# Kernel tuning notes

Hardware: AMD Instinct MI355X
Metric: run time of the kernel (lower is better)

## Reference

```python
import jax, jax.numpy as jnp
import numpy as np

N = 4096
NFEAT = 1024
NHID = 512
NCLS = 32
NLAYERS = 3
SPARSITY = 0.002


def _l2norm(x, eps=1e-12):
    n = jnp.sqrt(jnp.sum(x * x, axis=1, keepdims=True))
    return x / jnp.maximum(n, eps)


def setup_inputs() -> dict:
    key = jax.random.key(0)
    ks = jax.random.split(key, 12)
    # sparse-valued dense adjacency (original stores torch.sparse but densifies every hop)
    vals = jax.random.uniform(ks[0], (N, N), dtype=jnp.float32)
    mask = jax.random.uniform(ks[1], (N, N)) < SPARSITY
    adj = jnp.where(mask, vals, 0.0)
    features = jax.random.normal(ks[2], (N, NFEAT), dtype=jnp.float32)
    # y is a one-hot label matrix [N, nclass]
    labels = jax.random.randint(ks[3], (N,), 0, NCLS)
    y = jax.nn.one_hot(labels, NCLS, dtype=jnp.float32)
    s = 0.02
    W0 = jax.random.normal(ks[4], (NFEAT + 3 * NCLS, NHID), dtype=jnp.float32) * s
    b0 = jnp.zeros((NHID,), jnp.float32)
    W1_0 = jax.random.normal(ks[5], (NHID + 3 * NCLS, NHID), dtype=jnp.float32) * s
    b1_0 = jnp.zeros((NHID,), jnp.float32)
    W1_1 = jax.random.normal(ks[6], (NHID + 3 * NCLS, NHID), dtype=jnp.float32) * s
    b1_1 = jnp.zeros((NHID,), jnp.float32)
    W2 = jax.random.normal(ks[7], (NFEAT + NHID, NCLS), dtype=jnp.float32) * s
    b2 = jnp.zeros((NCLS,), jnp.float32)
    alphas = jnp.ones((NLAYERS, 5), jnp.float32)
    return {
        "adj": adj, "features": features, "y": y,
        "W0": W0, "b0": b0, "W1_0": W1_0, "b1_0": b1_0,
        "W1_1": W1_1, "b1_1": b1_1, "W2": W2, "b2": b2,
        "alphas": alphas, "layer_norm": 1,
    }


def reference(adj, features, y, W0, b0, W1_0, b1_0, W1_1, b1_1, W2, b2, alphas, layer_norm):
    Ws = [(W0, b0), (W1_0, b1_0), (W1_1, b1_1)]
    initial_features = jax.lax.stop_gradient(features)  # .clone().detach()
    feats = features
    max_features = None
    pow_adj = adj  # persists across layers (faithful to original): hops adj, adj^2, adj^4
    for i in range(NLAYERS):
        mask_alpha = jax.nn.softmax(alphas[i], axis=0)
        for _ in range(i):
            pow_adj = adj @ pow_adj
        hop = pow_adj @ feats                                   # [N, d]
        dist = (pow_adj > 0).astype(adj.dtype)                  # binarized reachability
        y_out = dist @ y                                        # [N, c]
        y_in = dist.T @ y                                       # [N, c]
        y_all = y_in + y_out
        hop = mask_alpha[0] * hop
        y_out = mask_alpha[1] * y_out
        y_in = mask_alpha[2] * y_in
        y_all = mask_alpha[3] * y_all
        mat = jnp.concatenate([hop, y_out, y_in, y_all], axis=1)
        W, b = Ws[i]
        tmp = mat @ W + b
        if layer_norm:
            tmp = _l2norm(tmp)
        feats = tmp
        max_features = tmp if max_features is None else jnp.maximum(max_features, tmp)
    final_mat = jnp.concatenate([initial_features, max_features], axis=1)
    out = jax.nn.relu(final_mat)
    # dropout: eval mode (identity)
    out = out @ W2 + b2
    return jax.nn.log_softmax(out, axis=1)
```

## Files before the change

kernel.cpp:

```cpp
#include <hip/hip_runtime.h>
#include <hip/hip_bf16.h>
#include <math.h>

typedef unsigned long long u64;
typedef unsigned short ushort_t;
typedef float f32x4 __attribute__((ext_vector_type(4)));
typedef short s16x8 __attribute__((ext_vector_type(8)));

#define NN 4096
#define NF 1024
#define NH 512
#define NC 32
#define LDP 40

__device__ inline float bf2f(ushort_t u) {
    unsigned int v = ((unsigned int)u) << 16;
    return __uint_as_float(v);
}
__device__ inline ushort_t f2bf(float f) {
    __hip_bfloat16 h = __float2bfloat16(f);
    return *(ushort_t*)&h;
}

__device__ void role_build(int i, int l, const float* __restrict__ adj,
                           u64* __restrict__ B1, int* __restrict__ rowcnt,
                           int* __restrict__ colidx, float* __restrict__ vals) {
    const float* row = adj + (size_t)i * NN + l * 64;
    const float4* row4 = (const float4*)row;
    u64 w = 0;
    #pragma unroll
    for (int k = 0; k < 16; ++k) {
        float4 v = row4[k];
        if (v.x > 0.f) w |= 1ULL << (4*k + 0);
        if (v.y > 0.f) w |= 1ULL << (4*k + 1);
        if (v.z > 0.f) w |= 1ULL << (4*k + 2);
        if (v.w > 0.f) w |= 1ULL << (4*k + 3);
    }
    B1[(size_t)i*64 + l] = w;
    int cnt = __popcll(w);
    int pre = cnt;
    #pragma unroll
    for (int o = 1; o < 64; o <<= 1) {
        int u = __shfl_up(pre, o, 64);
        if (l >= o) pre += u;
    }
    int excl = pre - cnt;
    int total = __shfl(pre, 63, 64);
    u64 ww = w;
    int idx = excl;
    while (ww) {
        int b = __ffsll((unsigned long long)ww) - 1;
        ww &= ww - 1;
        if (idx < 64) {
            colidx[i*64 + idx] = l*64 + b;
            vals[i*64 + idx] = row[b];
        }
        ++idx;
    }
    int tot = total < 64 ? total : 64;
    for (int s = tot + l; s < 64; s += 64) {
        colidx[i*64 + s] = 0;
        vals[i*64 + s] = 0.f;
    }
    if (l == 0) {
        int r8 = (tot + 7) & ~7;
        rowcnt[i] = r8 < 64 ? r8 : 64;
    }
}

__device__ void role_wt(const float* __restrict__ W, ushort_t* __restrict__ Wt,
                        int ksrc0, int Kd, int idx, char* smem, int t) {
    float (*tile)[33] = (float(*)[33])smem;
    int ktiles = Kd >> 5;
    int kb = (idx % ktiles) * 32, nb = (idx / ktiles) * 32;
    int tc = t & 31, tr8 = t >> 5;
    for (int r = tr8; r < 32; r += 8)
        tile[r][tc] = W[(size_t)(ksrc0 + kb + r) * NH + nb + tc];
    __syncthreads();
    for (int r = tr8; r < 32; r += 8)
        Wt[(size_t)(nb + r) * Kd + kb + tc] = f2bf(tile[tc][r]);
}

__device__ void role_bsq(int i, int t, char* smem, const u64* __restrict__ Bidx,
                         const u64* __restrict__ Bdat, u64* __restrict__ Bout) {
    u64* ridx = (u64*)smem;
    u64* part = ridx + 64;
    int wid = t >> 6, lane = t & 63;
    if (t < 64) ridx[t] = Bidx[(size_t)i*64 + t];
    __syncthreads();
    u64 acc = 0;
    for (int u = wid*16; u < wid*16 + 16; ++u) {
        u64 w = ridx[u];
        while (w) {
            int k = u*64 + (__ffsll((unsigned long long)w) - 1);
            w &= (w - 1);
            acc |= Bdat[(size_t)k*64 + lane];
        }
    }
    part[wid*64 + lane] = acc;
    __syncthreads();
    if (t < 64) Bout[(size_t)i*64 + t] = part[t] | part[64+t] | part[128+t] | part[192+t];
}

__device__ void role_btrans(int tb, int wid, int l, char* smem,
                            const u64* __restrict__ B, u64* __restrict__ BT) {
    u64* ld = ((u64*)smem) + wid*64;
    int I = tb >> 6, J = tb & 63;
    ld[l] = B[(size_t)(I*64 + l)*64 + J];
    __syncthreads();
    u64 out = 0;
    #pragma unroll
    for (int r = 0; r < 64; ++r) out |= ((ld[r] >> l) & 1ULL) << r;
    BT[(size_t)(J*64 + l)*64 + I] = out;
}

__device__ void role_ymat(int rb, int t, char* smem, const u64* __restrict__ B,
                          const u64* __restrict__ BT, const u64* __restrict__ LC,
                          const float* __restrict__ asp, ushort_t* __restrict__ yc) {
    u64* LCt   = (u64*)smem;
    u64* rows  = LCt + 64*32;
    u64* rowsT = rows + 8*64;
    for (int k = t; k < 2048; k += 256) {
        int c = k >> 6, w = k & 63;
        LCt[w*32 + c] = LC[k];
    }
    for (int k = t; k < 512; k += 256) {
        int r = k >> 6, w = k & 63;
        rows[r*64 + w]  = B[(size_t)(rb + r)*64 + w];
        rowsT[r*64 + w] = BT[(size_t)(rb + r)*64 + w];
    }
    __syncthreads();
    int wid = t >> 6, lane = t & 63;
    int h = lane >> 5, c = lane & 31;
    int r = wid * 2 + h;
    int co = 0, ci = 0;
    #pragma unroll
    for (int w = 0; w < 64; ++w) {
        u64 lc = LCt[w*32 + c];
        co += __popcll(rows[r*64 + w]  & lc);
        ci += __popcll(rowsT[r*64 + w] & lc);
    }
    float a1 = asp[1], a2 = asp[2], a3 = asp[3];
    size_t i = rb + r;
    yc[i*96 + c]      = f2bf(a1 * (float)co);
    yc[i*96 + 32 + c] = f2bf(a2 * (float)ci);
    yc[i*96 + 64 + c] = f2bf(a3 * (float)(co + ci));
}

__device__ void role_gemm(int bx, int tid, char* smem, const ushort_t* __restrict__ Abf,
                          const float* __restrict__ Af, int Ka,
                          const ushort_t* __restrict__ Bt, int K,
                          ushort_t* __restrict__ Cb, float* __restrict__ Cf) {
    ushort_t* As = (ushort_t*)smem;
    ushort_t* Bs = As + 64*LDP;
    int xcd = bx & 7, rest = bx >> 3;
    int nt = rest & 7, mt = (rest >> 3) * 8 + xcd;
    int bm = mt * 64, bn = nt * 64;
    int srow = tid >> 2, scol = (tid & 3) * 8;
    int wid = tid >> 6, lane = tid & 63;
    int fr = lane & 15, hi2 = lane >> 4, fk = hi2 * 8;
    f32x4 acc[4] = {{0,0,0,0},{0,0,0,0},{0,0,0,0},{0,0,0,0}};
    for (int k0 = 0; k0 < K; k0 += 32) {
        if (Abf) {
            *(s16x8*)&As[srow * LDP + scol] =
                *(const s16x8*)&Abf[(size_t)(bm + srow) * Ka + k0 + scol];
        } else {
            const float* ap = &Af[(size_t)(bm + srow) * Ka + k0 + scol];
            float4 a0 = *(const float4*)ap;
            float4 a1 = *(const float4*)(ap + 4);
            s16x8 o;
            o[0] = (short)f2bf(a0.x); o[1] = (short)f2bf(a0.y);
            o[2] = (short)f2bf(a0.z); o[3] = (short)f2bf(a0.w);
            o[4] = (short)f2bf(a1.x); o[5] = (short)f2bf(a1.y);
            o[6] = (short)f2bf(a1.z); o[7] = (short)f2bf(a1.w);
            *(s16x8*)&As[srow * LDP + scol] = o;
        }
        *(s16x8*)&Bs[srow * LDP + scol] =
            *(const s16x8*)&Bt[(size_t)(bn + srow) * K + k0 + scol];
        __syncthreads();
        s16x8 af = *(const s16x8*)&As[(wid * 16 + fr) * LDP + fk];
        #pragma unroll
        for (int j = 0; j < 4; ++j) {
            s16x8 bfv = *(const s16x8*)&Bs[(j * 16 + fr) * LDP + fk];
            acc[j] = __builtin_amdgcn_mfma_f32_16x16x32_bf16(af, bfv, acc[j], 0, 0, 0);
        }
        __syncthreads();
    }
    int drow = bm + wid * 16 + hi2 * 4;
    #pragma unroll
    for (int j = 0; j < 4; ++j) {
        int col = bn + j * 16 + fr;
        #pragma unroll
        for (int r = 0; r < 4; ++r) {
            if (Cb) Cb[(size_t)(drow + r) * NH + col] = f2bf(acc[j][r]);
            else    Cf[(size_t)(drow + r) * NH + col] = acc[j][r];
        }
    }
}

__device__ void role_spmm(int i, int lane, const int* __restrict__ rc,
                          const int* __restrict__ ci, const float* __restrict__ vl,
                          const ushort_t* __restrict__ X, ushort_t* __restrict__ Y) {
    int cnt = rc[i];
    float acc[8] = {0,0,0,0,0,0,0,0};
    for (int p = 0; p < cnt; p += 8) {
        int4   c0 = *(const int4*)&ci[i*64 + p];
        int4   c1 = *(const int4*)&ci[i*64 + p + 4];
        float4 v0 = *(const float4*)&vl[i*64 + p];
        float4 v1 = *(const float4*)&vl[i*64 + p + 4];
        s16x8 x0 = *(const s16x8*)&X[(size_t)c0.x * NH + 8*lane];
        s16x8 x1 = *(const s16x8*)&X[(size_t)c0.y * NH + 8*lane];
        s16x8 x2 = *(const s16x8*)&X[(size_t)c0.z * NH + 8*lane];
        s16x8 x3 = *(const s16x8*)&X[(size_t)c0.w * NH + 8*lane];
        s16x8 x4 = *(const s16x8*)&X[(size_t)c1.x * NH + 8*lane];
        s16x8 x5 = *(const s16x8*)&X[(size_t)c1.y * NH + 8*lane];
        s16x8 x6 = *(const s16x8*)&X[(size_t)c1.z * NH + 8*lane];
        s16x8 x7 = *(const s16x8*)&X[(size_t)c1.w * NH + 8*lane];
        #pragma unroll
        for (int j = 0; j < 8; ++j) {
            acc[j] += v0.x * bf2f((ushort_t)x0[j]);
            acc[j] += v0.y * bf2f((ushort_t)x1[j]);
            acc[j] += v0.z * bf2f((ushort_t)x2[j]);
            acc[j] += v0.w * bf2f((ushort_t)x3[j]);
            acc[j] += v1.x * bf2f((ushort_t)x4[j]);
            acc[j] += v1.y * bf2f((ushort_t)x5[j]);
            acc[j] += v1.z * bf2f((ushort_t)x6[j]);
            acc[j] += v1.w * bf2f((ushort_t)x7[j]);
        }
    }
    s16x8 o;
    #pragma unroll
    for (int j = 0; j < 8; ++j) o[j] = (short)f2bf(acc[j]);
    *(s16x8*)&Y[(size_t)i*NH + 8*lane] = o;
}

__device__ void role_spmmF(int i, int lane, const int* __restrict__ rc,
                           const int* __restrict__ ci, const float* __restrict__ vl,
                           const ushort_t* __restrict__ X, const float* __restrict__ yv,
                           const float* __restrict__ bias, int ln, float alpha,
                           ushort_t* __restrict__ F) {
    int cnt = rc[i];
    float acc[8] = {0,0,0,0,0,0,0,0};
    for (int p = 0; p < cnt; p += 8) {
        int4   c0 = *(const int4*)&ci[i*64 + p];
        int4   c1 = *(const int4*)&ci[i*64 + p + 4];
        float4 v0 = *(const float4*)&vl[i*64 + p];
        float4 v1 = *(const float4*)&vl[i*64 + p + 4];
        s16x8 x0 = *(const s16x8*)&X[(size_t)c0.x * NH + 8*lane];
        s16x8 x1 = *(const s16x8*)&X[(size_t)c0.y * NH + 8*lane];
        s16x8 x2 = *(const s16x8*)&X[(size_t)c0.z * NH + 8*lane];
        s16x8 x3 = *(const s16x8*)&X[(size_t)c0.w * NH + 8*lane];
        s16x8 x4 = *(const s16x8*)&X[(size_t)c1.x * NH + 8*lane];
        s16x8 x5 = *(const s16x8*)&X[(size_t)c1.y * NH + 8*lane];
        s16x8 x6 = *(const s16x8*)&X[(size_t)c1.z * NH + 8*lane];
        s16x8 x7 = *(const s16x8*)&X[(size_t)c1.w * NH + 8*lane];
        #pragma unroll
        for (int j = 0; j < 8; ++j) {
            acc[j] += v0.x * bf2f((ushort_t)x0[j]);
            acc[j] += v0.y * bf2f((ushort_t)x1[j]);
            acc[j] += v0.z * bf2f((ushort_t)x2[j]);
            acc[j] += v0.w * bf2f((ushort_t)x3[j]);
            acc[j] += v1.x * bf2f((ushort_t)x4[j]);
            acc[j] += v1.y * bf2f((ushort_t)x5[j]);
            acc[j] += v1.z * bf2f((ushort_t)x6[j]);
            acc[j] += v1.w * bf2f((ushort_t)x7[j]);
        }
    }
    const float* yr = yv + (size_t)i * NH + 8*lane;
    float4 ya = *(const float4*)yr;
    float4 yb = *(const float4*)(yr + 4);
    float4 ba = *(const float4*)&bias[8*lane];
    float4 bb = *(const float4*)&bias[8*lane + 4];
    float v[8];
    v[0] = alpha*acc[0] + ya.x + ba.x; v[1] = alpha*acc[1] + ya.y + ba.y;
    v[2] = alpha*acc[2] + ya.z + ba.z; v[3] = alpha*acc[3] + ya.w + ba.w;
    v[4] = alpha*acc[4] + yb.x + bb.x; v[5] = alpha*acc[5] + yb.y + bb.y;
    v[6] = alpha*acc[6] + yb.z + bb.z; v[7] = alpha*acc[7] + yb.w + bb.w;
    float ss = 0.f;
    #pragma unroll
    for (int j = 0; j < 8; ++j) ss += v[j]*v[j];
    #pragma unroll
    for (int o = 1; o < 64; o <<= 1) ss += __shfl_xor(ss, o, 64);
    float sc = ln ? 1.0f / fmaxf(sqrtf(ss), 1e-12f) : 1.0f;
    s16x8 o;
    #pragma unroll
    for (int j = 0; j < 8; ++j) o[j] = (short)f2bf(v[j] * sc);
    *(s16x8*)&F[(size_t)i*NH + 8*lane] = o;
}

__global__ __launch_bounds__(256) void k_setup(const float* __restrict__ adj,
        const float* __restrict__ features, ushort_t* __restrict__ featb,
        const float* __restrict__ y, u64* __restrict__ LC,
        const float* __restrict__ W0, const float* __restrict__ W1_0,
        const float* __restrict__ W1_1,
        ushort_t* __restrict__ Wh0t, ushort_t* __restrict__ Wy0t,
        ushort_t* __restrict__ Wh1t, ushort_t* __restrict__ Wy1t,
        ushort_t* __restrict__ Wh2t, ushort_t* __restrict__ Wy2t,
        const float* __restrict__ alphas, float* __restrict__ a_sm,
        u64* __restrict__ B1, int* __restrict__ rowcnt,
        int* __restrict__ colidx, float* __restrict__ vals) {
    __shared__ __align__(16) char smem[4352];
    int b = blockIdx.x, t = threadIdx.x;
    int wid = t >> 6, l = t & 63;
    if (b < 1024) {
        role_build(b*4 + wid, l, adj, B1, rowcnt, colidx, vals);
    } else if (b < 5120) {
        int base = (b - 1024) * 1024 + t * 4;
        float4 v = *(const float4*)&features[base];
        ushort4 o;
        o.x = f2bf(v.x); o.y = f2bf(v.y); o.z = f2bf(v.z); o.w = f2bf(v.w);
        *(ushort4*)&featb[base] = o;
    } else if (b < 5136) {
        int w = (b - 5120) * 4 + wid;
        const float* yr = y + (size_t)(w*64 + l) * NC;
        for (int c = 0; c < NC; ++c) {
            u64 m = __ballot(yr[c] > 0.5f);
            if (l == c) LC[c*64 + w] = m;
        }
    } else if (b < 5648) { role_wt(W0,   Wh0t, 0,    NF, b - 5136, smem, t); }
    else if (b < 5696)   { role_wt(W0,   Wy0t, NF,   96, b - 5648, smem, t); }
    else if (b < 5952)   { role_wt(W1_0, Wh1t, 0,    NH, b - 5696, smem, t); }
    else if (b < 6000)   { role_wt(W1_0, Wy1t, NH,   96, b - 5952, smem, t); }
    else if (b < 6256)   { role_wt(W1_1, Wh2t, 0,    NH, b - 6000, smem, t); }
    else if (b < 6304)   { role_wt(W1_1, Wy2t, NH,   96, b - 6256, smem, t); }
    else {
        if (t == 0) {
            for (int i = 0; i < 3; ++i) {
                float m = -1e30f;
                for (int j = 0; j < 5; ++j) m = fmaxf(m, alphas[i*5+j]);
                float e[5]; float s = 0.f;
                for (int j = 0; j < 5; ++j) { e[j] = expf(alphas[i*5+j] - m); s += e[j]; }
                for (int j = 0; j < 5; ++j) a_sm[i*5+j] = e[j] / s;
            }
        }
    }
}

__global__ __launch_bounds__(256) void k_p2(const ushort_t* __restrict__ featb,
        const ushort_t* __restrict__ Wh0t, ushort_t* __restrict__ zb,
        const u64* __restrict__ B1, u64* __restrict__ B2, u64* __restrict__ B1T) {
    __shared__ __align__(16) char smem[10240];
    int b = blockIdx.x, t = threadIdx.x;
    int wid = t >> 6, l = t & 63;
    if (b < 512)       role_gemm(b, t, smem, featb, nullptr, NF, Wh0t, NF, zb, nullptr);
    else if (b < 4608) role_bsq(b - 512, t, smem, B1, B1, B2);
    else               role_btrans((b - 4608)*4 + wid, wid, l, smem, B1, B1T);
}

__global__ __launch_bounds__(256) void k_p3(const u64* __restrict__ B1,
        const u64* __restrict__ B2, u64* __restrict__ B3, u64* __restrict__ B2T,
        const u64* __restrict__ B1T, const u64* __restrict__ LC,
        const float* __restrict__ a_sm, ushort_t* __restrict__ y0c) {
    __shared__ __align__(16) char smem[24576];
    int b = blockIdx.x, t = threadIdx.x;
    int wid = t >> 6, l = t & 63;
    if (b < 4096)      role_bsq(b, t, smem, B1, B2, B3);
    else if (b < 5120) role_btrans((b - 4096)*4 + wid, wid, l, smem, B2, B2T);
    else               role_ymat((b - 5120)*8, t, smem, B1, B1T, LC, a_sm, y0c);
}

__global__ __launch_bounds__(256) void k_p4(const ushort_t* __restrict__ y0c,
        const ushort_t* __restrict__ Wy0t, float* __restrict__ yv0,
        const u64* __restrict__ B2, const u64* __restrict__ B2T,
        const u64* __restrict__ LC, const float* __restrict__ a_sm,
        ushort_t* __restrict__ y1c,
        const u64* __restrict__ B1, const u64* __restrict__ B3, u64* __restrict__ B4) {
    __shared__ __align__(16) char smem[24576];
    int b = blockIdx.x, t = threadIdx.x;
    if (b < 512)       role_gemm(b, t, smem, y0c, nullptr, 96, Wy0t, 96, nullptr, yv0);
    else if (b < 1024) role_ymat((b - 512)*8, t, smem, B2, B2T, LC, a_sm + 5, y1c);
    else               role_bsq(b - 1024, t, smem, B1, B3, B4);
}

__global__ __launch_bounds__(256) void k_p5(const int* __restrict__ rc,
        const int* __restrict__ ci, const float* __restrict__ vl,
        const ushort_t* __restrict__ zb, const float* __restrict__ yv0,
        const float* __restrict__ b0, const int* __restrict__ lnflag,
        const float* __restrict__ a_sm, ushort_t* __restrict__ f1,
        const u64* __restrict__ B4, u64* __restrict__ B4T,
        const ushort_t* __restrict__ y1c, const ushort_t* __restrict__ Wy1t,
        float* __restrict__ yv1) {
    __shared__ __align__(16) char smem[10240];
    int b = blockIdx.x, t = threadIdx.x;
    int wid = t >> 6, l = t & 63;
    if (b < 1024)
        role_spmmF(b*4 + wid, l, rc, ci, vl, zb, yv0, b0, *lnflag, a_sm[0], f1);
    else if (b < 2048)
        role_btrans((b - 1024)*4 + wid, wid, l, smem, B4, B4T);
    else
        role_gemm(b - 2048, t, smem, y1c, nullptr, 96, Wy1t, 96, nullptr, yv1);
}

__global__ __launch_bounds__(256) void k_p6(const ushort_t* __restrict__ f1,
        const ushort_t* __restrict__ Wh1t, ushort_t* __restrict__ zb,
        const u64* __restrict__ B4, const u64* __restrict__ B4T,
        const u64* __restrict__ LC, const float* __restrict__ a_sm,
        ushort_t* __restrict__ y2c) {
    __shared__ __align__(16) char smem[24576];
    int b = blockIdx.x, t = threadIdx.x;
    if (b < 512) role_gemm(b, t, smem, f1, nullptr, NH, Wh1t, NH, zb, nullptr);
    else         role_ymat((b - 512)*8, t, smem, B4, B4T, LC, a_sm + 10, y2c);
}

__global__ __launch_bounds__(256) void k_p7(const int* __restrict__ rc,
        const int* __restrict__ ci, const float* __restrict__ vl,
        const ushort_t* __restrict__ zb, ushort_t* __restrict__ ub,
        const ushort_t* __restrict__ y2c, const ushort_t* __restrict__ Wy2t,
        float* __restrict__ yv2) {
    __shared__ __align__(16) char smem[10240];
    int b = blockIdx.x, t = threadIdx.x;
    int wid = t >> 6, l = t & 63;
    if (b < 1024) role_spmm(b*4 + wid, l, rc, ci, vl, zb, ub);
    else          role_gemm(b - 1024, t, smem, y2c, nullptr, 96, Wy2t, 96, nullptr, yv2);
}

__global__ __launch_bounds__(256) void k_spmm(const int* __restrict__ rc,
        const int* __restrict__ ci, const float* __restrict__ vl,
        const ushort_t* __restrict__ X, ushort_t* __restrict__ Y) {
    role_spmm(blockIdx.x*4 + (threadIdx.x >> 6), threadIdx.x & 63, rc, ci, vl, X, Y);
}

__global__ __launch_bounds__(256) void k_spmmF(const int* __restrict__ rc,
        const int* __restrict__ ci, const float* __restrict__ vl,
        const ushort_t* __restrict__ X, const float* __restrict__ yv,
        const float* __restrict__ bias, const int* __restrict__ lnflag,
        const float* __restrict__ a_sm, int ai, ushort_t* __restrict__ F) {
    role_spmmF(blockIdx.x*4 + (threadIdx.x >> 6), threadIdx.x & 63, rc, ci, vl,
               X, yv, bias, *lnflag, a_sm[ai], F);
}

__global__ __launch_bounds__(256) void k_gemmz(const ushort_t* __restrict__ A,
        const ushort_t* __restrict__ Bt, ushort_t* __restrict__ C, int K) {
    __shared__ __align__(16) char smem[10240];
    role_gemm(blockIdx.x, threadIdx.x, smem, A, nullptr, K, Bt, K, C, nullptr);
}

__global__ __launch_bounds__(256) void k_final(const ushort_t* __restrict__ featb,
        const ushort_t* __restrict__ f1, const ushort_t* __restrict__ f2,
        const ushort_t* __restrict__ f3, const float* __restrict__ W2,
        const float* __restrict__ b2, float* __restrict__ out) {
    int rb = blockIdx.x * 8;
    int t = threadIdx.x;
    __shared__ float rows[8][NF + NH];
    __shared__ float part[8][8][32];
    #pragma unroll
    for (int r = 0; r < 8; ++r) {
        ushort4 v = *(const ushort4*)&featb[(size_t)(rb + r) * NF + t * 4];
        rows[r][t*4+0] = fmaxf(bf2f(v.x), 0.f);
        rows[r][t*4+1] = fmaxf(bf2f(v.y), 0.f);
        rows[r][t*4+2] = fmaxf(bf2f(v.z), 0.f);
        rows[r][t*4+3] = fmaxf(bf2f(v.w), 0.f);
    }
    #pragma unroll
    for (int q = 0; q < 2; ++q) {
        int ch = t*2 + q;
        int rr = ch >> 6, k8 = (ch & 63) * 8;
        s16x8 a = *(const s16x8*)&f1[(size_t)(rb + rr)*NH + k8];
        s16x8 bq = *(const s16x8*)&f2[(size_t)(rb + rr)*NH + k8];
        s16x8 cq = *(const s16x8*)&f3[(size_t)(rb + rr)*NH + k8];
        #pragma unroll
        for (int j = 0; j < 8; ++j) {
            float m = fmaxf(fmaxf(bf2f((ushort_t)a[j]), bf2f((ushort_t)bq[j])),
                            bf2f((ushort_t)cq[j]));
            rows[rr][NF + k8 + j] = fmaxf(m, 0.f);
        }
    }
    __syncthreads();
    int c = t & 31, g = t >> 5;
    float acc[8] = {0,0,0,0,0,0,0,0};
    for (int k = g * 192; k < (g + 1) * 192; ++k) {
        float w = W2[(size_t)k * NC + c];
        #pragma unroll
        for (int r = 0; r < 8; ++r) acc[r] += rows[r][k] * w;
    }
    #pragma unroll
    for (int r = 0; r < 8; ++r) part[g][r][c] = acc[r];
    __syncthreads();
    int r = g;
    float lg = b2[c];
    #pragma unroll
    for (int gg = 0; gg < 8; ++gg) lg += part[gg][r][c];
    float m = lg;
    #pragma unroll
    for (int o = 16; o > 0; o >>= 1) m = fmaxf(m, __shfl_xor(m, o, 32));
    float e = expf(lg - m), s = e;
    #pragma unroll
    for (int o = 16; o > 0; o >>= 1) s += __shfl_xor(s, o, 32);
    out[(size_t)(rb + r) * NC + c] = lg - m - logf(s);
}

extern "C" void kernel_launch(void* const* d_in, const int* in_sizes, int n_in,
                              void* d_out, int out_size, void* d_ws, size_t ws_size,
                              hipStream_t stream) {
    const float* adj      = (const float*)d_in[0];
    const float* features = (const float*)d_in[1];
    const float* y        = (const float*)d_in[2];
    const float* W0       = (const float*)d_in[3];
    const float* b0       = (const float*)d_in[4];
    const float* W1_0     = (const float*)d_in[5];
    const float* b1_0     = (const float*)d_in[6];
    const float* W1_1     = (const float*)d_in[7];
    const float* b1_1     = (const float*)d_in[8];
    const float* W2       = (const float*)d_in[9];
    const float* b2       = (const float*)d_in[10];
    const float* alphas   = (const float*)d_in[11];
    const int*   lnflag   = (const int*)d_in[12];
    float* out = (float*)d_out;

    char* ws = (char*)d_ws;
    size_t off = 0;
    auto alloc = [&](size_t bytes) -> char* {
        char* p = ws + off;
        off = (off + bytes + 255) & ~(size_t)255;
        return p;
    };
    float* a_sm   = (float*)alloc(16 * 4);
    int*   rowcnt = (int*)alloc((size_t)NN * 4);
    int*   colidx = (int*)alloc((size_t)NN * 64 * 4);
    float* vals   = (float*)alloc((size_t)NN * 64 * 4);
    u64* B1  = (u64*)alloc((size_t)NN * 64 * 8);
    u64* B2  = (u64*)alloc((size_t)NN * 64 * 8);
    u64* B3  = (u64*)alloc((size_t)NN * 64 * 8);
    u64* B4  = (u64*)alloc((size_t)NN * 64 * 8);
    u64* B1T = (u64*)alloc((size_t)NN * 64 * 8);
    u64* B2T = (u64*)alloc((size_t)NN * 64 * 8);
    u64* B4T = (u64*)alloc((size_t)NN * 64 * 8);
    u64* LC  = (u64*)alloc((size_t)NC * 64 * 8);
    ushort_t* featb = (ushort_t*)alloc((size_t)NN * NF * 2);
    ushort_t* Wh0t = (ushort_t*)alloc((size_t)NH * NF * 2);
    ushort_t* Wh1t = (ushort_t*)alloc((size_t)NH * NH * 2);
    ushort_t* Wh2t = (ushort_t*)alloc((size_t)NH * NH * 2);
    ushort_t* Wy0t = (ushort_t*)alloc((size_t)NH * 96 * 2);
    ushort_t* Wy1t = (ushort_t*)alloc((size_t)NH * 96 * 2);
    ushort_t* Wy2t = (ushort_t*)alloc((size_t)NH * 96 * 2);
    ushort_t* y0c  = (ushort_t*)alloc((size_t)NN * 96 * 2);
    ushort_t* y1c  = (ushort_t*)alloc((size_t)NN * 96 * 2);
    ushort_t* y2c  = (ushort_t*)alloc((size_t)NN * 96 * 2);
    float* yv0 = (float*)alloc((size_t)NN * NH * 4);
    float* yv1 = (float*)alloc((size_t)NN * NH * 4);
    float* yv2 = (float*)alloc((size_t)NN * NH * 4);
    ushort_t* zb = (ushort_t*)alloc((size_t)NN * NH * 2);
    ushort_t* ub = (ushort_t*)alloc((size_t)NN * NH * 2);
    ushort_t* vb = (ushort_t*)alloc((size_t)NN * NH * 2);
    ushort_t* f1 = (ushort_t*)alloc((size_t)NN * NH * 2);
    ushort_t* f2 = (ushort_t*)alloc((size_t)NN * NH * 2);
    ushort_t* f3 = (ushort_t*)alloc((size_t)NN * NH * 2);

    k_setup<<<6305, 256, 0, stream>>>(adj, features, featb, y, LC, W0, W1_0, W1_1,
                                      Wh0t, Wy0t, Wh1t, Wy1t, Wh2t, Wy2t,
                                      alphas, a_sm, B1, rowcnt, colidx, vals);
    k_p2<<<5632, 256, 0, stream>>>(featb, Wh0t, zb, B1, B2, B1T);
    k_p3<<<5632, 256, 0, stream>>>(B1, B2, B3, B2T, B1T, LC, a_sm, y0c);
    k_p4<<<5120, 256, 0, stream>>>(y0c, Wy0t, yv0, B2, B2T, LC, a_sm, y1c, B1, B3, B4);
    k_p5<<<2560, 256, 0, stream>>>(rowcnt, colidx, vals, zb, yv0, b0, lnflag, a_sm,
                                   f1, B4, B4T, y1c, Wy1t, yv1);
    k_p6<<<1024, 256, 0, stream>>>(f1, Wh1t, zb, B4, B4T, LC, a_sm, y2c);
    k_p7<<<1536, 256, 0, stream>>>(rowcnt, colidx, vals, zb, ub, y2c, Wy2t, yv2);
    k_spmmF<<<1024, 256, 0, stream>>>(rowcnt, colidx, vals, ub, yv1, b1_0, lnflag,
                                      a_sm, 5, f2);
    k_gemmz<<<512, 256, 0, stream>>>(f2, Wh2t, zb, NH);
    k_spmm<<<1024, 256, 0, stream>>>(rowcnt, colidx, vals, zb, ub);
    k_spmm<<<1024, 256, 0, stream>>>(rowcnt, colidx, vals, ub, vb);
    k_spmm<<<1024, 256, 0, stream>>>(rowcnt, colidx, vals, vb, ub);
    k_spmmF<<<1024, 256, 0, stream>>>(rowcnt, colidx, vals, ub, yv2, b1_1, lnflag,
                                      a_sm, 10, f3);
    k_final<<<512, 256, 0, stream>>>(featb, f1, f2, f3, W2, b2, out);
}
```

Baseline: 186.2 us.

## Fuse pairs of sparse hops into two-hop gather kernels

Replaces consecutive single-hop SpMM passes with a two-hop kernel that walks neighbours of neighbours directly, computing A·(A·X) without writing the intermediate to memory. Layer 1's hop plus finalize goes from two launches to one merged into k_p7, and layer 2's four hops go from four launches to two. This removes intermediate bf16 round-trips and launches. In exchange each row does about deg² gathers serialised over the inner loop with less parallelism, and the intermediate is no longer rounded to bf16. A true per-row count is stored so the outer loop skips padding entries.

```diff
diff --git a/kernel.cpp b/kernel.cpp
--- a/kernel.cpp
+++ b/kernel.cpp
@@ -24,6 +24,7 @@
 
 __device__ void role_build(int i, int l, const float* __restrict__ adj,
                            u64* __restrict__ B1, int* __restrict__ rowcnt,
+                           int* __restrict__ rowcnt_true,
                            int* __restrict__ colidx, float* __restrict__ vals) {
     const float* row = adj + (size_t)i * NN + l * 64;
     const float4* row4 = (const float4*)row;
@@ -63,6 +64,7 @@
         vals[i*64 + s] = 0.f;
     }
     if (l == 0) {
+        rowcnt_true[i] = tot;
         int r8 = (tot + 7) & ~7;
         rowcnt[i] = r8 < 64 ? r8 : 64;
     }
@@ -196,42 +198,6 @@
             else    Cf[(size_t)(drow + r) * NH + col] = acc[j][r];
         }
     }
-}
-
-__device__ void role_spmm(int i, int lane, const int* __restrict__ rc,
-                          const int* __restrict__ ci, const float* __restrict__ vl,
-                          const ushort_t* __restrict__ X, ushort_t* __restrict__ Y) {
-    int cnt = rc[i];
-    float acc[8] = {0,0,0,0,0,0,0,0};
-    for (int p = 0; p < cnt; p += 8) {
-        int4   c0 = *(const int4*)&ci[i*64 + p];
-        int4   c1 = *(const int4*)&ci[i*64 + p + 4];
-        float4 v0 = *(const float4*)&vl[i*64 + p];
-        float4 v1 = *(const float4*)&vl[i*64 + p + 4];
-        s16x8 x0 = *(const s16x8*)&X[(size_t)c0.x * NH + 8*lane];
-        s16x8 x1 = *(const s16x8*)&X[(size_t)c0.y * NH + 8*lane];
-        s16x8 x2 = *(const s16x8*)&X[(size_t)c0.z * NH + 8*lane];
-        s16x8 x3 = *(const s16x8*)&X[(size_t)c0.w * NH + 8*lane];
-        s16x8 x4 = *(const s16x8*)&X[(size_t)c1.x * NH + 8*lane];
-        s16x8 x5 = *(const s16x8*)&X[(size_t)c1.y * NH + 8*lane];
-        s16x8 x6 = *(const s16x8*)&X[(size_t)c1.z * NH + 8*lane];
-        s16x8 x7 = *(const s16x8*)&X[(size_t)c1.w * NH + 8*lane];
-        #pragma unroll
-        for (int j = 0; j < 8; ++j) {
-            acc[j] += v0.x * bf2f((ushort_t)x0[j]);
-            acc[j] += v0.y * bf2f((ushort_t)x1[j]);
-            acc[j] += v0.z * bf2f((ushort_t)x2[j]);
-            acc[j] += v0.w * bf2f((ushort_t)x3[j]);
-            acc[j] += v1.x * bf2f((ushort_t)x4[j]);
-            acc[j] += v1.y * bf2f((ushort_t)x5[j]);
-            acc[j] += v1.z * bf2f((ushort_t)x6[j]);
-            acc[j] += v1.w * bf2f((ushort_t)x7[j]);
-        }
-    }
-    s16x8 o;
-    #pragma unroll
-    for (int j = 0; j < 8; ++j) o[j] = (short)f2bf(acc[j]);
-    *(s16x8*)&Y[(size_t)i*NH + 8*lane] = o;
 }
 
 __device__ void role_spmmF(int i, int lane, const int* __restrict__ rc,
@@ -288,6 +254,87 @@
     *(s16x8*)&F[(size_t)i*NH + 8*lane] = o;
 }
 
+__device__ void role_dh2(int i, int lane, const int* __restrict__ rc8,
+                         const int* __restrict__ rct,
+                         const int* __restrict__ ci, const float* __restrict__ vl,
+                         const ushort_t* __restrict__ X, float* __restrict__ acc) {
+    int cti = rct[i];
+    for (int p = 0; p < cti; ++p) {
+        int j = ci[i*64 + p];
+        float vij = vl[i*64 + p];
+        int cj = rc8[j];
+        for (int q = 0; q < cj; q += 8) {
+            int4   c0 = *(const int4*)&ci[j*64 + q];
+            int4   c1 = *(const int4*)&ci[j*64 + q + 4];
+            float4 v0 = *(const float4*)&vl[j*64 + q];
+            float4 v1 = *(const float4*)&vl[j*64 + q + 4];
+            float w0 = vij*v0.x, w1 = vij*v0.y, w2 = vij*v0.z, w3 = vij*v0.w;
+            float w4 = vij*v1.x, w5 = vij*v1.y, w6 = vij*v1.z, w7 = vij*v1.w;
+            s16x8 x0 = *(const s16x8*)&X[(size_t)c0.x * NH + 8*lane];
+            s16x8 x1 = *(const s16x8*)&X[(size_t)c0.y * NH + 8*lane];
+            s16x8 x2 = *(const s16x8*)&X[(size_t)c0.z * NH + 8*lane];
+            s16x8 x3 = *(const s16x8*)&X[(size_t)c0.w * NH + 8*lane];
+            s16x8 x4 = *(const s16x8*)&X[(size_t)c1.x * NH + 8*lane];
+            s16x8 x5 = *(const s16x8*)&X[(size_t)c1.y * NH + 8*lane];
+            s16x8 x6 = *(const s16x8*)&X[(size_t)c1.z * NH + 8*lane];
+            s16x8 x7 = *(const s16x8*)&X[(size_t)c1.w * NH + 8*lane];
+            #pragma unroll
+            for (int jj = 0; jj < 8; ++jj) {
+                acc[jj] += w0 * bf2f((ushort_t)x0[jj]);
+                acc[jj] += w1 * bf2f((ushort_t)x1[jj]);
+                acc[jj] += w2 * bf2f((ushort_t)x2[jj]);
+                acc[jj] += w3 * bf2f((ushort_t)x3[jj]);
+                acc[jj] += w4 * bf2f((ushort_t)x4[jj]);
+                acc[jj] += w5 * bf2f((ushort_t)x5[jj]);
+                acc[jj] += w6 * bf2f((ushort_t)x6[jj]);
+                acc[jj] += w7 * bf2f((ushort_t)x7[jj]);
+            }
+        }
+    }
+}
+
+__device__ void role_dh2P(int i, int lane, const int* __restrict__ rc8,
+                          const int* __restrict__ rct,
+                          const int* __restrict__ ci, const float* __restrict__ vl,
+                          const ushort_t* __restrict__ X, ushort_t* __restrict__ Y) {
+    float acc[8] = {0,0,0,0,0,0,0,0};
+    role_dh2(i, lane, rc8, rct, ci, vl, X, acc);
+    s16x8 o;
+    #pragma unroll
+    for (int j = 0; j < 8; ++j) o[j] = (short)f2bf(acc[j]);
+    *(s16x8*)&Y[(size_t)i*NH + 8*lane] = o;
+}
+
+__device__ void role_dh2F(int i, int lane, const int* __restrict__ rc8,
+                          const int* __restrict__ rct,
+                          const int* __restrict__ ci, const float* __restrict__ vl,
+                          const ushort_t* __restrict__ X, const float* __restrict__ yv,
+                          const float* __restrict__ bias, int ln, float alpha,
+                          ushort_t* __restrict__ F) {
+    float acc[8] = {0,0,0,0,0,0,0,0};
+    role_dh2(i, lane, rc8, rct, ci, vl, X, acc);
+    const float* yr = yv + (size_t)i * NH + 8*lane;
+    float4 ya = *(const float4*)yr;
+    float4 yb = *(const float4*)(yr + 4);
+    float4 ba = *(const float4*)&bias[8*lane];
+    float4 bb = *(const float4*)&bias[8*lane + 4];
+    float v[8];
+    v[0] = alpha*acc[0] + ya.x + ba.x; v[1] = alpha*acc[1] + ya.y + ba.y;
+    v[2] = alpha*acc[2] + ya.z + ba.z; v[3] = alpha*acc[3] + ya.w + ba.w;
+    v[4] = alpha*acc[4] + yb.x + bb.x; v[5] = alpha*acc[5] + yb.y + bb.y;
+    v[6] = alpha*acc[6] + yb.z + bb.z; v[7] = alpha*acc[7] + yb.w + bb.w;
+    float ss = 0.f;
+    #pragma unroll
+    for (int j = 0; j < 8; ++j) ss += v[j]*v[j];
+    #pragma unroll
+    for (int o = 1; o < 64; o <<= 1) ss += __shfl_xor(ss, o, 64);
+    float sc = ln ? 1.0f / fmaxf(sqrtf(ss), 1e-12f) : 1.0f;
+    s16x8 o;
+    #pragma unroll
+    for (int j = 0; j < 8; ++j) o[j] = (short)f2bf(v[j] * sc);
+    *(s16x8*)&F[(size_t)i*NH + 8*lane] = o;
+}
+
 __global__ __launch_bounds__(256) void k_setup(const float* __restrict__ adj,
         const float* __restrict__ features, ushort_t* __restrict__ featb,
         const float* __restrict__ y, u64* __restrict__ LC,
@@ -297,13 +344,13 @@
         ushort_t* __restrict__ Wh1t, ushort_t* __restrict__ Wy1t,
         ushort_t* __restrict__ Wh2t, ushort_t* __restrict__ Wy2t,
         const float* __restrict__ alphas, float* __restrict__ a_sm,
-        u64* __restrict__ B1, int* __restrict__ rowcnt,
+        u64* __restrict__ B1, int* __restrict__ rowcnt, int* __restrict__ rowcnt_true,
         int* __restrict__ colidx, float* __restrict__ vals) {
     __shared__ __align__(16) char smem[4352];
     int b = blockIdx.x, t = threadIdx.x;
     int wid = t >> 6, l = t & 63;
     if (b < 1024) {
-        role_build(b*4 + wid, l, adj, B1, rowcnt, colidx, vals);
+        role_build(b*4 + wid, l, adj, B1, rowcnt, rowcnt_true, colidx, vals);
     } else if (b < 5120) {
         int base = (b - 1024) * 1024 + t * 4;
         float4 v = *(const float4*)&features[base];
@@ -402,37 +449,44 @@
     else         role_ymat((b - 512)*8, t, smem, B4, B4T, LC, a_sm + 10, y2c);
 }
 
-__global__ __launch_bounds__(256) void k_p7(const int* __restrict__ rc,
+__global__ __launch_bounds__(256) void k_p7(const int* __restrict__ rc8,
+        const int* __restrict__ rct,
         const int* __restrict__ ci, const float* __restrict__ vl,
-        const ushort_t* __restrict__ zb, ushort_t* __restrict__ ub,
+        const ushort_t* __restrict__ zb, const float* __restrict__ yv1,
+        const float* __restrict__ b1_0, const int* __restrict__ lnflag,
+        const float* __restrict__ a_sm, ushort_t* __restrict__ f2,
         const ushort_t* __restrict__ y2c, const ushort_t* __restrict__ Wy2t,
         float* __restrict__ yv2) {
     __shared__ __align__(16) char smem[10240];
     int b = blockIdx.x, t = threadIdx.x;
     int wid = t >> 6, l = t & 63;
-    if (b < 1024) role_spmm(b*4 + wid, l, rc, ci, vl, zb, ub);
-    else          role_gemm(b - 1024, t, smem, y2c, nullptr, 96, Wy2t, 96, nullptr, yv2);
-}
-
-__global__ __launch_bounds__(256) void k_spmm(const int* __restrict__ rc,
+    if (b < 1024)
+        role_dh2F(b*4 + wid, l, rc8, rct, ci, vl, zb, yv1, b1_0, *lnflag, a_sm[5], f2);
+    else
+        role_gemm(b - 1024, t, smem, y2c, nullptr, 96, Wy2t, 96, nullptr, yv2);
+}
+
+__global__ __launch_bounds__(256) void k_gemmz(const ushort_t* __restrict__ A,
+        const ushort_t* __restrict__ Bt, ushort_t* __restrict__ C, int K) {
+    __shared__ __align__(16) char smem[10240];
+    role_gemm(blockIdx.x, threadIdx.x, smem, A, nullptr, K, Bt, K, C, nullptr);
+}
+
+__global__ __launch_bounds__(256) void k_dh(const int* __restrict__ rc8,
+        const int* __restrict__ rct,
         const int* __restrict__ ci, const float* __restrict__ vl,
         const ushort_t* __restrict__ X, ushort_t* __restrict__ Y) {
-    role_spmm(blockIdx.x*4 + (threadIdx.x >> 6), threadIdx.x & 63, rc, ci, vl, X, Y);
-}
-
-__global__ __launch_bounds__(256) void k_spmmF(const int* __restrict__ rc,
+    role_dh2P(blockIdx.x*4 + (threadIdx.x >> 6), threadIdx.x & 63, rc8, rct, ci, vl, X, Y);
+}
+
+__global__ __launch_bounds__(256) void k_dhF(const int* __restrict__ rc8,
+        const int* __restrict__ rct,
         const int* __restrict__ ci, const float* __restrict__ vl,
         const ushort_t* __restrict__ X, const float* __restrict__ yv,
         const float* __restrict__ bias, const int* __restrict__ lnflag,
         const float* __restrict__ a_sm, int ai, ushort_t* __restrict__ F) {
-    role_spmmF(blockIdx.x*4 + (threadIdx.x >> 6), threadIdx.x & 63, rc, ci, vl,
-               X, yv, bias, *lnflag, a_sm[ai], F);
-}
-
-__global__ __launch_bounds__(256) void k_gemmz(const ushort_t* __restrict__ A,
-        const ushort_t* __restrict__ Bt, ushort_t* __restrict__ C, int K) {
-    __shared__ __align__(16) char smem[10240];
-    role_gemm(blockIdx.x, threadIdx.x, smem, A, nullptr, K, Bt, K, C, nullptr);
+    role_dh2F(blockIdx.x*4 + (threadIdx.x >> 6), threadIdx.x & 63, rc8, rct, ci, vl,
+              X, yv, bias, *lnflag, a_sm[ai], F);
 }
 
 __global__ __launch_bounds__(256) void k_final(const ushort_t* __restrict__ featb,
@@ -514,10 +568,11 @@
         off = (off + bytes + 255) & ~(size_t)255;
         return p;
     };
-    float* a_sm   = (float*)alloc(16 * 4);
-    int*   rowcnt = (int*)alloc((size_t)NN * 4);
-    int*   colidx = (int*)alloc((size_t)NN * 64 * 4);
-    float* vals   = (float*)alloc((size_t)NN * 64 * 4);
+    float* a_sm        = (float*)alloc(16 * 4);
+    int*   rowcnt      = (int*)alloc((size_t)NN * 4);
+    int*   rowcnt_true = (int*)alloc((size_t)NN * 4);
+    int*   colidx      = (int*)alloc((size_t)NN * 64 * 4);
+    float* vals        = (float*)alloc((size_t)NN * 64 * 4);
     u64* B1  = (u64*)alloc((size_t)NN * 64 * 8);
     u64* B2  = (u64*)alloc((size_t)NN * 64 * 8);
     u64* B3  = (u64*)alloc((size_t)NN * 64 * 8);
@@ -541,28 +596,25 @@
     float* yv2 = (float*)alloc((size_t)NN * NH * 4);
     ushort_t* zb = (ushort_t*)alloc((size_t)NN * NH * 2);
     ushort_t* ub = (ushort_t*)alloc((size_t)NN * NH * 2);
-    ushort_t* vb = (ushort_t*)alloc((size_t)NN * NH * 2);
     ushort_t* f1 = (ushort_t*)alloc((size_t)NN * NH * 2);
     ushort_t* f2 = (ushort_t*)alloc((size_t)NN * NH * 2);
     ushort_t* f3 = (ushort_t*)alloc((size_t)NN * NH * 2);
 
     k_setup<<<6305, 256, 0, stream>>>(adj, features, featb, y, LC, W0, W1_0, W1_1,
                                       Wh0t, Wy0t, Wh1t, Wy1t, Wh2t, Wy2t,
-                                      alphas, a_sm, B1, rowcnt, colidx, vals);
+                                      alphas, a_sm, B1, rowcnt, rowcnt_true,
+                                      colidx, vals);
     k_p2<<<5632, 256, 0, stream>>>(featb, Wh0t, zb, B1, B2, B1T);
     k_p3<<<5632, 256, 0, stream>>>(B1, B2, B3, B2T, B1T, LC, a_sm, y0c);
     k_p4<<<5120, 256, 0, stream>>>(y0c, Wy0t, yv0, B2, B2T, LC, a_sm, y1c, B1, B3, B4);
     k_p5<<<2560, 256, 0, stream>>>(rowcnt, colidx, vals, zb, yv0, b0, lnflag, a_sm,
                                    f1, B4, B4T, y1c, Wy1t, yv1);
     k_p6<<<1024, 256, 0, stream>>>(f1, Wh1t, zb, B4, B4T, LC, a_sm, y2c);
-    k_p7<<<1536, 256, 0, stream>>>(rowcnt, colidx, vals, zb, ub, y2c, Wy2t, yv2);
-    k_spmmF<<<1024, 256, 0, stream>>>(rowcnt, colidx, vals, ub, yv1, b1_0, lnflag,
-                                      a_sm, 5, f2);
+    k_p7<<<1536, 256, 0, stream>>>(rowcnt, rowcnt_true, colidx, vals, zb, yv1, b1_0,
+                                   lnflag, a_sm, f2, y2c, Wy2t, yv2);
     k_gemmz<<<512, 256, 0, stream>>>(f2, Wh2t, zb, NH);
-    k_spmm<<<1024, 256, 0, stream>>>(rowcnt, colidx, vals, zb, ub);
-    k_spmm<<<1024, 256, 0, stream>>>(rowcnt, colidx, vals, ub, vb);
-    k_spmm<<<1024, 256, 0, stream>>>(rowcnt, colidx, vals, vb, ub);
-    k_spmmF<<<1024, 256, 0, stream>>>(rowcnt, colidx, vals, ub, yv2, b1_1, lnflag,
-                                      a_sm, 10, f3);
+    k_dh<<<1024, 256, 0, stream>>>(rowcnt, rowcnt_true, colidx, vals, zb, ub);
+    k_dhF<<<1024, 256, 0, stream>>>(rowcnt, rowcnt_true, colidx, vals, ub, yv2, b1_1,
+                                    lnflag, a_sm, 10, f3);
     k_final<<<512, 256, 0, stream>>>(featb, f1, f2, f3, W2, b2, out);
 }
```

New measurement: 250.0 us. 34.2% more time.
